# Kernel optimization log

Hardware: AMD Instinct MI355X
Metric: run time of the kernel (lower is better)

## Reference

```python
import math
import jax, jax.numpy as jnp
import numpy as np

NTYPE, C, H, E = 3, 256, 8, 32  # n_embd=256, n_head=8, edge_dim=32
A1 = 16  # aux_x1 feature dim (aux_x2 dim = E - A1)


def setup_inputs() -> dict:
    key = jax.random.key(0)
    ks = jax.random.split(key, 16)
    B, T1, T2 = 8, 128, 256
    s = 0.02
    return {
        "x1": jax.random.normal(ks[0], (B, T1, C), jnp.float32),
        "x2": jax.random.normal(ks[1], (B, T2, C), jnp.float32),
        "aux_x1": jax.random.normal(ks[2], (B, T1, A1), jnp.float32),
        "aux_x2": jax.random.normal(ks[3], (B, T2, E - A1), jnp.float32),
        "masks": jax.random.randint(ks[4], (NTYPE, B, T1, T2), 0, 2, jnp.int32),
        # per-type linear params, stored (in, out) so y = x @ W + b
        "Wq": jax.random.normal(ks[5], (NTYPE, C, C), jnp.float32) * s,
        "bq": jnp.zeros((NTYPE, C), jnp.float32),
        "Wk": jax.random.normal(ks[6], (NTYPE, C + E, C), jnp.float32) * s,
        "bk": jnp.zeros((NTYPE, C), jnp.float32),
        "Wv": jax.random.normal(ks[7], (NTYPE, C + E, C), jnp.float32) * s,
        "bv": jnp.zeros((NTYPE, C), jnp.float32),
        "Wp": jax.random.normal(ks[8], (NTYPE, C, C), jnp.float32) * s,
        "bp": jnp.zeros((NTYPE, C), jnp.float32),
    }


def _aux_attn(x1, x2, aux_x1, aux_x2, mask, Wq, bq, Wk, bk, Wv, bv, Wp, bp):
    """One AuxCrossAttention type. mask: (B,T1,T2) int."""
    B, T1, _ = x1.shape
    T2 = x2.shape[1]
    hd = C // H
    scale = 1.0 / math.sqrt(hd)

    q = x1 @ Wq + bq  # (B,T1,C)
    # k/v over aug_x2 = [x2 | aux_x1 | aux_x2]; split the linear instead of
    # materializing the (B,T1,T2,C+E) concat (same math by linearity).
    Wk_x, Wk_a1, Wk_a2 = Wk[:C], Wk[C:C + A1], Wk[C + A1:]
    Wv_x, Wv_a1, Wv_a2 = Wv[:C], Wv[C:C + A1], Wv[C + A1:]
    k = (x2 @ Wk_x + aux_x2 @ Wk_a2 + bk)[:, None] + (aux_x1 @ Wk_a1)[:, :, None]  # (B,T1,T2,C)
    v = (x2 @ Wv_x + aux_x2 @ Wv_a2 + bv)[:, None] + (aux_x1 @ Wv_a1)[:, :, None]  # (B,T1,T2,C)

    qh = q.reshape(B, T1, H, hd)
    kh = k.reshape(B, T1, T2, H, hd)
    vh = v.reshape(B, T1, T2, H, hd)

    att = jnp.einsum("bthd,btshd->bhts", qh, kh) * scale  # (B,H,T1,T2)
    valid = (mask != 0)[:, None]  # (B,1,T1,T2)
    att = jnp.where(valid, att, -jnp.inf)
    all_masked = (mask == 0).all(-1)  # (B,T1)
    att = jnp.where(all_masked[:, None, :, None], 0.0, att)
    f = jnp.finfo(att.dtype)
    att = jnp.nan_to_num(att, nan=0.0, posinf=f.max, neginf=f.min)
    att = jax.nn.softmax(att, axis=-1)

    y = jnp.einsum("bhts,btshd->bthd", att, vh).reshape(B, T1, C)
    return y @ Wp + bp


def reference(x1, x2, aux_x1, aux_x2, masks, Wq, bq, Wk, bk, Wv, bv, Wp, bp):
    resid = jnp.zeros_like(x1)
    for i in range(NTYPE):
        resid = resid + _aux_attn(x1, x2, aux_x1, aux_x2, masks[i],
                                  Wq[i], bq[i], Wk[i], bk[i], Wv[i], bv[i], Wp[i], bp[i])
    return resid
```

## Files before the change

kernel.cpp:

```cpp
#include <hip/hip_runtime.h>
#include <hip/hip_bf16.h>

#define NC 256
#define HD 32

typedef __attribute__((ext_vector_type(8))) short short8;
typedef __attribute__((ext_vector_type(4))) short short4v;
typedef __attribute__((ext_vector_type(4))) float f32x4;

#define QSC (0.17677669529663687f * 1.4426950408889634f)

__device__ __forceinline__ unsigned short f2bf(float f) {
    union { float f; unsigned u; } v; v.f = f;
    unsigned r = v.u + 0x7fffu + ((v.u >> 16) & 1u);
    return (unsigned short)(r >> 16);
}
__device__ __forceinline__ short8 cvt8(float4 a, float4 b) {
    short8 s;
    s[0] = (short)f2bf(a.x); s[1] = (short)f2bf(a.y);
    s[2] = (short)f2bf(a.z); s[3] = (short)f2bf(a.w);
    s[4] = (short)f2bf(b.x); s[5] = (short)f2bf(b.y);
    s[6] = (short)f2bf(b.z); s[7] = (short)f2bf(b.w);
    return s;
}

__global__ __launch_bounds__(256) void prep(
    const float* __restrict__ x1, const float* __restrict__ x2,
    const float* __restrict__ ax1, const float* __restrict__ ax2,
    const int* __restrict__ masks,
    const float* __restrict__ Wq, const float* __restrict__ Wk,
    const float* __restrict__ Wv, const float* __restrict__ Wp,
    short* __restrict__ x1b, short* __restrict__ A2, short* __restrict__ ax1p,
    unsigned int* __restrict__ mb,
    short* __restrict__ WqT, short* __restrict__ WkT, short* __restrict__ WvT,
    short* __restrict__ WpT)
{
    const int bx = blockIdx.x, tid = threadIdx.x;
    const short8 zero8 = {0, 0, 0, 0, 0, 0, 0, 0};

    if (bx < 64) {
        const size_t base = ((size_t)bx * 256 + tid) * 16;
        const float* p = x1 + base;
        float4 a = *(const float4*)p,       b = *(const float4*)(p + 4);
        float4 c = *(const float4*)(p + 8), d = *(const float4*)(p + 12);
        *(short8*)&x1b[base]     = cvt8(a, b);
        *(short8*)&x1b[base + 8] = cvt8(c, d);
    } else if (bx < 352) {
        const int g = (bx - 64) * 256 + tid;
        const int row = g / 36, c8 = g - row * 36;
        short8 s;
        if (c8 < 32) {
            const float* p = x2 + (size_t)row * 256 + c8 * 8;
            s = cvt8(*(const float4*)p, *(const float4*)(p + 4));
        } else if (c8 < 34) {
            const float* p = ax2 + (size_t)row * 16 + (c8 - 32) * 8;
            s = cvt8(*(const float4*)p, *(const float4*)(p + 4));
        } else {
            s = zero8;
        }
        *(short8*)&A2[(size_t)row * 288 + c8 * 8] = s;
    } else if (bx < 356) {
        const int row = (bx - 352) * 256 + tid;
        const float* p = ax1 + (size_t)row * 16;
        float4 a = *(const float4*)p,       b = *(const float4*)(p + 4);
        float4 c = *(const float4*)(p + 8), d = *(const float4*)(p + 12);
        short* o = ax1p + (size_t)row * 32;
        *(short8*)o        = cvt8(a, b);
        *(short8*)(o + 8)  = cvt8(c, d);
        *(short8*)(o + 16) = zero8;
        *(short8*)(o + 24) = zero8;
    } else if (bx < 548) {
        const int r0 = (bx - 356) * 16;
        const int wave = tid >> 6, lane = tid & 63;
        for (int rr = 0; rr < 16; ++rr) {
            const int row = r0 + rr;
            const int mk = masks[(size_t)row * 256 + tid];
            unsigned long long bal = __ballot(mk != 0);
            if (lane == 0) {
                mb[row * 8 + wave * 2 + 0] = (unsigned int)bal;
                mb[row * 8 + wave * 2 + 1] = (unsigned int)(bal >> 32);
            }
        }
    } else if (bx < 644) {
        const int idx = bx - 548, i = idx >> 5, k8 = idx & 31;
        const int n = tid;
        const float* W = Wq + (size_t)i * 256 * 256;
        short8 s;
#pragma unroll
        for (int j = 0; j < 8; ++j) s[j] = (short)f2bf(W[(size_t)(k8 * 8 + j) * 256 + n]);
        *(short8*)&WqT[(size_t)i * 256 * 256 + (size_t)n * 256 + k8 * 8] = s;
    } else if (bx < 860) {
        const int idx0 = bx - 644;
        const int kv = idx0 / 108, idx = idx0 % 108;
        const int i = idx / 36, k8 = idx % 36;
        const int n = tid;
        const float* W = (kv ? Wv : Wk) + (size_t)i * 288 * 256;
        short* O = (kv ? WvT : WkT) + (size_t)i * 256 * 288;
        short8 s;
#pragma unroll
        for (int j = 0; j < 8; ++j) {
            const int kp = k8 * 8 + j;
            const int src = (kp < 256) ? kp : (kp < 272 ? kp + 16 : -1);
            s[j] = (src >= 0) ? (short)f2bf(W[(size_t)src * 256 + n]) : (short)0;
        }
        *(short8*)&O[(size_t)n * 288 + k8 * 8] = s;
    } else {
        const int idx = bx - 860, i = idx >> 5, k8 = idx & 31;
        const int n = tid;
        const float* W = Wp + (size_t)i * 256 * 256;
        short8 s;
#pragma unroll
        for (int j = 0; j < 8; ++j) s[j] = (short)f2bf(W[(size_t)(k8 * 8 + j) * 256 + n]);
        *(short8*)&WpT[(size_t)i * 256 * 256 + (size_t)n * 256 + k8 * 8] = s;
    }
}

__global__ __launch_bounds__(1024) void qkv_attn(
    const short* __restrict__ x1b, const short* __restrict__ A2,
    const short* __restrict__ WqT, const short* __restrict__ WkT,
    const short* __restrict__ WvT, const float* __restrict__ Wv,
    const short* __restrict__ WpT,
    const float* __restrict__ bq, const float* __restrict__ bk,
    const float* __restrict__ bv, const unsigned int* __restrict__ mb,
    short* __restrict__ yb, short* __restrict__ WeffT)
{
    const int tid = threadIdx.x;
    const int wave = tid >> 6, lane = tid & 63;
    const int qd = lane >> 4, ml = lane & 15;
    const int bx = blockIdx.x;

    if (bx >= 192) {
        if (wave != 0) return;
        const int wb = bx - 192;
        const int n = wb * 16 + ml;
        f32x4 acc = {0.f, 0.f, 0.f, 0.f};
        for (int i = 0; i < 3; ++i) {
            const float* Wvp = Wv + (size_t)i * 288 * 256;
            const short* Wpt = WpT + (size_t)i * 256 * 256;
#pragma unroll
            for (int step = 0; step < 8; ++step) {
                const float* ap = Wvp + (size_t)(256 + ml) * 256 + step * 32 + qd * 8;
                short8 af = cvt8(*(const float4*)ap, *(const float4*)(ap + 4));
                short8 bf = *(const short8*)&Wpt[(size_t)n * 256 + step * 32 + qd * 8];
                acc = __builtin_amdgcn_mfma_f32_16x16x32_bf16(af, bf, acc, 0, 0, 0);
            }
        }
#pragma unroll
        for (int r = 0; r < 4; ++r) {
            WeffT[n * 32 + qd * 4 + r] = (short)f2bf(acc[r]);
            WeffT[n * 32 + 16 + qd * 4 + r] = 0;
        }
        return;
    }

    const int i = bx >> 6, b = (bx >> 3) & 7, h = bx & 7;
    const size_t bb = (size_t)i * 8 + b;
    const int hc = h * 32;

    __shared__ short q_s[128][40];
    __shared__ short k_s[256][40];
    __shared__ short vT_s[32][264];
    __shared__ short P_s[8][1024];

    const short* Wq_i = WqT + (size_t)i * 256 * 256;
    const short* Wk_i = WkT + (size_t)i * 256 * 288;
    const short* Wv_i = WvT + (size_t)i * 256 * 288;

    f32x4 qacc[2], kacc[2], vacc[2];
#pragma unroll
    for (int nt = 0; nt < 2; ++nt) {
        qacc[nt] = {0.f, 0.f, 0.f, 0.f};
        kacc[nt] = {0.f, 0.f, 0.f, 0.f};
        vacc[nt] = {0.f, 0.f, 0.f, 0.f};
    }

    for (int step = 0; step < 8; ++step) {
        short8 afq, bfq[2], af, bfk[2], bfv[2];
        if (wave < 8) {
            afq = *(const short8*)&x1b[(size_t)(b * 128 + wave * 16 + ml) * 256 + step * 32 + qd * 8];
#pragma unroll
            for (int nt = 0; nt < 2; ++nt)
                bfq[nt] = *(const short8*)&Wq_i[(size_t)(hc + nt * 16 + ml) * 256 + step * 32 + qd * 8];
        }
        af = *(const short8*)&A2[(size_t)(b * 256 + wave * 16 + ml) * 288 + step * 32 + qd * 8];
#pragma unroll
        for (int nt = 0; nt < 2; ++nt) {
            bfk[nt] = *(const short8*)&Wk_i[(size_t)(hc + nt * 16 + ml) * 288 + step * 32 + qd * 8];
            bfv[nt] = *(const short8*)&Wv_i[(size_t)(hc + nt * 16 + ml) * 288 + step * 32 + qd * 8];
        }
        if (wave < 8) {
#pragma unroll
            for (int nt = 0; nt < 2; ++nt)
                qacc[nt] = __builtin_amdgcn_mfma_f32_16x16x32_bf16(afq, bfq[nt], qacc[nt], 0, 0, 0);
        }
#pragma unroll
        for (int nt = 0; nt < 2; ++nt) {
            kacc[nt] = __builtin_amdgcn_mfma_f32_16x16x32_bf16(af, bfk[nt], kacc[nt], 0, 0, 0);
            vacc[nt] = __builtin_amdgcn_mfma_f32_16x16x32_bf16(af, bfv[nt], vacc[nt], 0, 0, 0);
        }
    }
    {
        const int step = 8;
        short8 af, bfk[2], bfv[2];
        af = *(const short8*)&A2[(size_t)(b * 256 + wave * 16 + ml) * 288 + step * 32 + qd * 8];
#pragma unroll
        for (int nt = 0; nt < 2; ++nt) {
            bfk[nt] = *(const short8*)&Wk_i[(size_t)(hc + nt * 16 + ml) * 288 + step * 32 + qd * 8];
            bfv[nt] = *(const short8*)&Wv_i[(size_t)(hc + nt * 16 + ml) * 288 + step * 32 + qd * 8];
        }
#pragma unroll
        for (int nt = 0; nt < 2; ++nt) {
            kacc[nt] = __builtin_amdgcn_mfma_f32_16x16x32_bf16(af, bfk[nt], kacc[nt], 0, 0, 0);
            vacc[nt] = __builtin_amdgcn_mfma_f32_16x16x32_bf16(af, bfv[nt], vacc[nt], 0, 0, 0);
        }
    }

    if (wave < 8) {
#pragma unroll
        for (int nt = 0; nt < 2; ++nt) {
            const float bsq = bq[i * 256 + hc + nt * 16 + ml];
            const int r0 = wave * 16 + qd * 4;
#pragma unroll
            for (int r = 0; r < 4; ++r)
                q_s[r0 + r][nt * 16 + ml] = (short)f2bf((qacc[nt][r] + bsq) * QSC);
        }
    }
#pragma unroll
    for (int nt = 0; nt < 2; ++nt) {
        const float bsk = bk[i * 256 + hc + nt * 16 + ml];
        const float bsvv = bv[i * 256 + hc + nt * 16 + ml];
        const int s0 = wave * 16 + qd * 4;
#pragma unroll
        for (int r = 0; r < 4; ++r)
            k_s[s0 + r][nt * 16 + ml] = (short)f2bf(kacc[nt][r] + bsk);
        short4v s;
        s.x = (short)f2bf(vacc[nt][0] + bsvv);
        s.y = (short)f2bf(vacc[nt][1] + bsvv);
        s.z = (short)f2bf(vacc[nt][2] + bsvv);
        s.w = (short)f2bf(vacc[nt][3] + bsvv);
        *(short4v*)&vT_s[nt * 16 + ml][s0] = s;
    }
    __syncthreads();

    if (wave >= 8) return;
    short* Pw = &P_s[wave][0];
    {
        const int t0 = wave * 16;
        const int tb = t0 + qd * 4;

        uint4 wlo[4], whi[4];
#pragma unroll
        for (int r = 0; r < 4; ++r) {
            const unsigned int* p = mb + (bb * 128 + tb + r) * 8;
            wlo[r] = *(const uint4*)p;
            whi[r] = *(const uint4*)(p + 4);
        }

        short8 af = *(const short8*)&q_s[t0 + ml][qd * 8];

        f32x4 sacc[16];
#pragma unroll
        for (int nt = 0; nt < 16; ++nt) sacc[nt] = {0.f, 0.f, 0.f, 0.f};
#pragma unroll
        for (int nt = 0; nt < 16; ++nt) {
            short8 bf = *(const short8*)&k_s[nt * 16 + ml][qd * 8];
            sacc[nt] = __builtin_amdgcn_mfma_f32_16x16x32_bf16(af, bf, sacc[nt], 0, 0, 0);
        }

        f32x4 rs = {0.f, 0.f, 0.f, 0.f};
#pragma unroll
        for (int nt = 0; nt < 16; ++nt) {
#pragma unroll
            for (int r = 0; r < 4; ++r) {
                unsigned int w;
                switch (nt >> 1) {
                    case 0: w = wlo[r].x; break; case 1: w = wlo[r].y; break;
                    case 2: w = wlo[r].z; break; case 3: w = wlo[r].w; break;
                    case 4: w = whi[r].x; break; case 5: w = whi[r].y; break;
                    case 6: w = whi[r].z; break; default: w = whi[r].w; break;
                }
                const bool mk = (w >> ((nt & 1) * 16 + ml)) & 1u;
                float e = mk ? __builtin_amdgcn_exp2f(sacc[nt][r]) : 0.f;
                sacc[nt][r] = e;
                rs[r] += e;
            }
        }
#pragma unroll
        for (int off = 1; off <= 8; off <<= 1) {
#pragma unroll
            for (int r = 0; r < 4; ++r) rs[r] += __shfl_xor(rs[r], off);
        }
        f32x4 pinv, pfill;
#pragma unroll
        for (int r = 0; r < 4; ++r) {
            const bool z = (rs[r] == 0.f);
            pinv[r]  = z ? 0.f : 1.f / rs[r];
            pfill[r] = z ? (1.f / 256.f) : 0.f;
        }

        f32x4 oacc[2];
        oacc[0] = {0.f, 0.f, 0.f, 0.f};
        oacc[1] = {0.f, 0.f, 0.f, 0.f};
#pragma unroll
        for (int quar = 0; quar < 4; ++quar) {
#pragma unroll
            for (int nt4 = 0; nt4 < 4; ++nt4) {
                const int nt = quar * 4 + nt4;
                const int sgrp = 2 * nt4 + (ml >> 3);
                const int pos = ml & 7;
#pragma unroll
                for (int r = 0; r < 4; ++r) {
                    const float p = sacc[nt][r] * pinv[r] + pfill[r];
                    Pw[(sgrp * 16 + qd * 4 + r) * 8 + pos] = (short)f2bf(p);
                }
            }
#pragma unroll
            for (int ksl = 0; ksl < 2; ++ksl) {
                const int ks = quar * 2 + ksl;
                short8 pa = *(const short8*)&Pw[((ksl * 4 + qd) * 16 + ml) * 8];
#pragma unroll
                for (int n2 = 0; n2 < 2; ++n2) {
                    short8 vf = *(const short8*)&vT_s[n2 * 16 + ml][ks * 32 + qd * 8];
                    oacc[n2] = __builtin_amdgcn_mfma_f32_16x16x32_bf16(pa, vf, oacc[n2], 0, 0, 0);
                }
            }
        }

#pragma unroll
        for (int n2 = 0; n2 < 2; ++n2) {
            const int d = hc + n2 * 16 + ml;
#pragma unroll
            for (int r = 0; r < 4; ++r)
                yb[(size_t)(bb * 128 + tb + r) * 256 + d] = (short)f2bf(oacc[n2][r]);
        }
    }
}

__global__ __launch_bounds__(256) void proj2(
    const short* __restrict__ yb, const short* __restrict__ WpT,
    const short* __restrict__ ax1p, const short* __restrict__ WeffT,
    const float* __restrict__ bp, float* __restrict__ out)
{
    const int bx = blockIdx.x;
    const int m0 = (bx >> 2) * 16, n0 = (bx & 3) * 64;
    const int tid = threadIdx.x;
    const int wave = tid >> 6, lane = tid & 63;
    const int qd = lane >> 4, ml = lane & 15;
    const int col = n0 + wave * 16 + ml;

    f32x4 acc = {0.f, 0.f, 0.f, 0.f};

#pragma unroll
    for (int i = 0; i < 3; ++i) {
        const short* A = yb + (size_t)i * 1024 * 256;
        const short* W = WpT + (size_t)i * 256 * 256;
#pragma unroll
        for (int step = 0; step < 8; ++step) {
            short8 af = *(const short8*)&A[(size_t)(m0 + ml) * 256 + step * 32 + qd * 8];
            short8 bf = *(const short8*)&W[(size_t)col * 256 + step * 32 + qd * 8];
            acc = __builtin_amdgcn_mfma_f32_16x16x32_bf16(af, bf, acc, 0, 0, 0);
        }
    }
    {
        short8 af = *(const short8*)&ax1p[(size_t)(m0 + ml) * 32 + qd * 8];
        short8 bf = *(const short8*)&WeffT[(size_t)col * 32 + qd * 8];
        acc = __builtin_amdgcn_mfma_f32_16x16x32_bf16(af, bf, acc, 0, 0, 0);
    }
    const float b3 = bp[col] + bp[256 + col] + bp[512 + col];
    const int row0 = m0 + qd * 4;
#pragma unroll
    for (int r = 0; r < 4; ++r)
        out[(size_t)(row0 + r) * 256 + col] = acc[r] + b3;
}

extern "C" void kernel_launch(void* const* d_in, const int* in_sizes, int n_in,
                              void* d_out, int out_size, void* d_ws, size_t ws_size,
                              hipStream_t stream)
{
    const float* x1  = (const float*)d_in[0];
    const float* x2  = (const float*)d_in[1];
    const float* ax1 = (const float*)d_in[2];
    const float* ax2 = (const float*)d_in[3];
    const int*   mk  = (const int*)d_in[4];
    const float* Wq  = (const float*)d_in[5];
    const float* bq  = (const float*)d_in[6];
    const float* Wk  = (const float*)d_in[7];
    const float* bk  = (const float*)d_in[8];
    const float* Wv  = (const float*)d_in[9];
    const float* bv  = (const float*)d_in[10];
    const float* Wp  = (const float*)d_in[11];
    const float* bp  = (const float*)d_in[12];

    char* w = (char*)d_ws;
    short* x1b   = (short*)(w + 0);
    short* A2    = (short*)(w + 524288);
    short* ax1p  = (short*)(w + 1703936);
    short* WqT   = (short*)(w + 1769472);
    short* WkT   = (short*)(w + 2162688);
    short* WvT   = (short*)(w + 2605056);
    short* WpT   = (short*)(w + 3047424);
    unsigned int* mbits = (unsigned int*)(w + 3440640);
    short* WeffT = (short*)(w + 3538944);
    short* yb    = (short*)(w + 3555328);

    prep<<<dim3(956), 256, 0, stream>>>(x1, x2, ax1, ax2, mk, Wq, Wk, Wv, Wp,
                                        x1b, A2, ax1p, mbits, WqT, WkT, WvT, WpT);
    qkv_attn<<<dim3(208), 1024, 0, stream>>>(x1b, A2, WqT, WkT, WvT, Wv, WpT,
                                             bq, bk, bv, mbits, yb, WeffT);
    proj2<<<dim3(256), 256, 0, stream>>>(yb, WpT, ax1p, WeffT, bp, (float*)d_out);
}
```

Measured before the change: 116.5 us.

## Fuse fp32-to-bf16 conversion of activations and Q/K/V weights into qkv_attn

```diff
diff --git a/kernel.cpp b/kernel.cpp
--- a/kernel.cpp
+++ b/kernel.cpp
@@ -23,44 +23,54 @@
     s[6] = (short)f2bf(b.z); s[7] = (short)f2bf(b.w);
     return s;
 }
+__device__ __forceinline__ short8 wfrag(const float* __restrict__ W, int k0, int n) {
+    short8 s;
+#pragma unroll
+    for (int j = 0; j < 8; ++j) s[j] = (short)f2bf(W[(size_t)(k0 + j) * 256 + n]);
+    return s;
+}
+__device__ __forceinline__ short8 wfrag288(const float* __restrict__ W, int k0, int n) {
+    short8 s;
+#pragma unroll
+    for (int j = 0; j < 8; ++j) {
+        const int kp = k0 + j;
+        const int src = (kp < 256) ? kp : (kp < 272 ? kp + 16 : -1);
+        s[j] = (src >= 0) ? (short)f2bf(W[(size_t)src * 256 + n]) : (short)0;
+    }
+    return s;
+}
 
 __global__ __launch_bounds__(256) void prep(
-    const float* __restrict__ x1, const float* __restrict__ x2,
-    const float* __restrict__ ax1, const float* __restrict__ ax2,
-    const int* __restrict__ masks,
-    const float* __restrict__ Wq, const float* __restrict__ Wk,
-    const float* __restrict__ Wv, const float* __restrict__ Wp,
-    short* __restrict__ x1b, short* __restrict__ A2, short* __restrict__ ax1p,
-    unsigned int* __restrict__ mb,
-    short* __restrict__ WqT, short* __restrict__ WkT, short* __restrict__ WvT,
-    short* __restrict__ WpT)
+    const int* __restrict__ masks, const float* __restrict__ Wp,
+    const float* __restrict__ ax1,
+    unsigned int* __restrict__ mb, short* __restrict__ WpT,
+    short* __restrict__ ax1p)
 {
     const int bx = blockIdx.x, tid = threadIdx.x;
     const short8 zero8 = {0, 0, 0, 0, 0, 0, 0, 0};
 
-    if (bx < 64) {
-        const size_t base = ((size_t)bx * 256 + tid) * 16;
-        const float* p = x1 + base;
-        float4 a = *(const float4*)p,       b = *(const float4*)(p + 4);
-        float4 c = *(const float4*)(p + 8), d = *(const float4*)(p + 12);
-        *(short8*)&x1b[base]     = cvt8(a, b);
-        *(short8*)&x1b[base + 8] = cvt8(c, d);
-    } else if (bx < 352) {
-        const int g = (bx - 64) * 256 + tid;
-        const int row = g / 36, c8 = g - row * 36;
+    if (bx < 192) {
+        const int r0 = bx * 16;
+        const int wave = tid >> 6, lane = tid & 63;
+        for (int rr = 0; rr < 16; ++rr) {
+            const int row = r0 + rr;
+            const int mk = masks[(size_t)row * 256 + tid];
+            unsigned long long bal = __ballot(mk != 0);
+            if (lane == 0) {
+                mb[row * 8 + wave * 2 + 0] = (unsigned int)bal;
+                mb[row * 8 + wave * 2 + 1] = (unsigned int)(bal >> 32);
+            }
+        }
+    } else if (bx < 288) {
+        const int idx = bx - 192, i = idx >> 5, k8 = idx & 31;
+        const int n = tid;
+        const float* W = Wp + (size_t)i * 256 * 256;
         short8 s;
-        if (c8 < 32) {
-            const float* p = x2 + (size_t)row * 256 + c8 * 8;
-            s = cvt8(*(const float4*)p, *(const float4*)(p + 4));
-        } else if (c8 < 34) {
-            const float* p = ax2 + (size_t)row * 16 + (c8 - 32) * 8;
-            s = cvt8(*(const float4*)p, *(const float4*)(p + 4));
-        } else {
-            s = zero8;
-        }
-        *(short8*)&A2[(size_t)row * 288 + c8 * 8] = s;
-    } else if (bx < 356) {
-        const int row = (bx - 352) * 256 + tid;
+#pragma unroll
+        for (int j = 0; j < 8; ++j) s[j] = (short)f2bf(W[(size_t)(k8 * 8 + j) * 256 + n]);
+        *(short8*)&WpT[(size_t)i * 256 * 256 + (size_t)n * 256 + k8 * 8] = s;
+    } else {
+        const int row = (bx - 288) * 256 + tid;
         const float* p = ax1 + (size_t)row * 16;
         float4 a = *(const float4*)p,       b = *(const float4*)(p + 4);
         float4 c = *(const float4*)(p + 8), d = *(const float4*)(p + 12);
@@ -69,57 +79,14 @@
         *(short8*)(o + 8)  = cvt8(c, d);
         *(short8*)(o + 16) = zero8;
         *(short8*)(o + 24) = zero8;
-    } else if (bx < 548) {
-        const int r0 = (bx - 356) * 16;
-        const int wave = tid >> 6, lane = tid & 63;
-        for (int rr = 0; rr < 16; ++rr) {
-            const int row = r0 + rr;
-            const int mk = masks[(size_t)row * 256 + tid];
-            unsigned long long bal = __ballot(mk != 0);
-            if (lane == 0) {
-                mb[row * 8 + wave * 2 + 0] = (unsigned int)bal;
-                mb[row * 8 + wave * 2 + 1] = (unsigned int)(bal >> 32);
-            }
-        }
-    } else if (bx < 644) {
-        const int idx = bx - 548, i = idx >> 5, k8 = idx & 31;
-        const int n = tid;
-        const float* W = Wq + (size_t)i * 256 * 256;
-        short8 s;
-#pragma unroll
-        for (int j = 0; j < 8; ++j) s[j] = (short)f2bf(W[(size_t)(k8 * 8 + j) * 256 + n]);
-        *(short8*)&WqT[(size_t)i * 256 * 256 + (size_t)n * 256 + k8 * 8] = s;
-    } else if (bx < 860) {
-        const int idx0 = bx - 644;
-        const int kv = idx0 / 108, idx = idx0 % 108;
-        const int i = idx / 36, k8 = idx % 36;
-        const int n = tid;
-        const float* W = (kv ? Wv : Wk) + (size_t)i * 288 * 256;
-        short* O = (kv ? WvT : WkT) + (size_t)i * 256 * 288;
-        short8 s;
-#pragma unroll
-        for (int j = 0; j < 8; ++j) {
-            const int kp = k8 * 8 + j;
-            const int src = (kp < 256) ? kp : (kp < 272 ? kp + 16 : -1);
-            s[j] = (src >= 0) ? (short)f2bf(W[(size_t)src * 256 + n]) : (short)0;
-        }
-        *(short8*)&O[(size_t)n * 288 + k8 * 8] = s;
-    } else {
-        const int idx = bx - 860, i = idx >> 5, k8 = idx & 31;
-        const int n = tid;
-        const float* W = Wp + (size_t)i * 256 * 256;
-        short8 s;
-#pragma unroll
-        for (int j = 0; j < 8; ++j) s[j] = (short)f2bf(W[(size_t)(k8 * 8 + j) * 256 + n]);
-        *(short8*)&WpT[(size_t)i * 256 * 256 + (size_t)n * 256 + k8 * 8] = s;
     }
 }
 
 __global__ __launch_bounds__(1024) void qkv_attn(
-    const short* __restrict__ x1b, const short* __restrict__ A2,
-    const short* __restrict__ WqT, const short* __restrict__ WkT,
-    const short* __restrict__ WvT, const float* __restrict__ Wv,
-    const short* __restrict__ WpT,
+    const float* __restrict__ x1, const float* __restrict__ x2,
+    const float* __restrict__ ax2,
+    const float* __restrict__ Wq, const float* __restrict__ Wk,
+    const float* __restrict__ Wv, const short* __restrict__ WpT,
     const float* __restrict__ bq, const float* __restrict__ bk,
     const float* __restrict__ bv, const unsigned int* __restrict__ mb,
     short* __restrict__ yb, short* __restrict__ WeffT)
@@ -128,6 +95,7 @@
     const int wave = tid >> 6, lane = tid & 63;
     const int qd = lane >> 4, ml = lane & 15;
     const int bx = blockIdx.x;
+    const short8 zero8 = {0, 0, 0, 0, 0, 0, 0, 0};
 
     if (bx >= 192) {
         if (wave != 0) return;
@@ -162,9 +130,9 @@
     __shared__ short vT_s[32][264];
     __shared__ short P_s[8][1024];
 
-    const short* Wq_i = WqT + (size_t)i * 256 * 256;
-    const short* Wk_i = WkT + (size_t)i * 256 * 288;
-    const short* Wv_i = WvT + (size_t)i * 256 * 288;
+    const float* Wq_i = Wq + (size_t)i * 256 * 256;
+    const float* Wk_i = Wk + (size_t)i * 288 * 256;
+    const float* Wv_i = Wv + (size_t)i * 288 * 256;
 
     f32x4 qacc[2], kacc[2], vacc[2];
 #pragma unroll
@@ -175,18 +143,23 @@
     }
 
     for (int step = 0; step < 8; ++step) {
+        const int k0 = step * 32 + qd * 8;
         short8 afq, bfq[2], af, bfk[2], bfv[2];
         if (wave < 8) {
-            afq = *(const short8*)&x1b[(size_t)(b * 128 + wave * 16 + ml) * 256 + step * 32 + qd * 8];
+            const float* px = x1 + (size_t)(b * 128 + wave * 16 + ml) * 256 + k0;
+            afq = cvt8(*(const float4*)px, *(const float4*)(px + 4));
 #pragma unroll
             for (int nt = 0; nt < 2; ++nt)
-                bfq[nt] = *(const short8*)&Wq_i[(size_t)(hc + nt * 16 + ml) * 256 + step * 32 + qd * 8];
-        }
-        af = *(const short8*)&A2[(size_t)(b * 256 + wave * 16 + ml) * 288 + step * 32 + qd * 8];
-#pragma unroll
-        for (int nt = 0; nt < 2; ++nt) {
-            bfk[nt] = *(const short8*)&Wk_i[(size_t)(hc + nt * 16 + ml) * 288 + step * 32 + qd * 8];
-            bfv[nt] = *(const short8*)&Wv_i[(size_t)(hc + nt * 16 + ml) * 288 + step * 32 + qd * 8];
+                bfq[nt] = wfrag(Wq_i, k0, hc + nt * 16 + ml);
+        }
+        {
+            const float* pa = x2 + (size_t)(b * 256 + wave * 16 + ml) * 256 + k0;
+            af = cvt8(*(const float4*)pa, *(const float4*)(pa + 4));
+        }
+#pragma unroll
+        for (int nt = 0; nt < 2; ++nt) {
+            bfk[nt] = wfrag288(Wk_i, k0, hc + nt * 16 + ml);
+            bfv[nt] = wfrag288(Wv_i, k0, hc + nt * 16 + ml);
         }
         if (wave < 8) {
 #pragma unroll
@@ -200,13 +173,18 @@
         }
     }
     {
-        const int step = 8;
+        const int k0 = 256 + qd * 8;
         short8 af, bfk[2], bfv[2];
-        af = *(const short8*)&A2[(size_t)(b * 256 + wave * 16 + ml) * 288 + step * 32 + qd * 8];
-#pragma unroll
-        for (int nt = 0; nt < 2; ++nt) {
-            bfk[nt] = *(const short8*)&Wk_i[(size_t)(hc + nt * 16 + ml) * 288 + step * 32 + qd * 8];
-            bfv[nt] = *(const short8*)&Wv_i[(size_t)(hc + nt * 16 + ml) * 288 + step * 32 + qd * 8];
+        if (qd < 2) {
+            const float* pa = ax2 + (size_t)(b * 256 + wave * 16 + ml) * 16 + qd * 8;
+            af = cvt8(*(const float4*)pa, *(const float4*)(pa + 4));
+        } else {
+            af = zero8;
+        }
+#pragma unroll
+        for (int nt = 0; nt < 2; ++nt) {
+            bfk[nt] = wfrag288(Wk_i, k0, hc + nt * 16 + ml);
+            bfv[nt] = wfrag288(Wv_i, k0, hc + nt * 16 + ml);
         }
 #pragma unroll
         for (int nt = 0; nt < 2; ++nt) {
@@ -392,20 +370,14 @@
     const float* bp  = (const float*)d_in[12];
 
     char* w = (char*)d_ws;
-    short* x1b   = (short*)(w + 0);
-    short* A2    = (short*)(w + 524288);
     short* ax1p  = (short*)(w + 1703936);
-    short* WqT   = (short*)(w + 1769472);
-    short* WkT   = (short*)(w + 2162688);
-    short* WvT   = (short*)(w + 2605056);
     short* WpT   = (short*)(w + 3047424);
     unsigned int* mbits = (unsigned int*)(w + 3440640);
     short* WeffT = (short*)(w + 3538944);
     short* yb    = (short*)(w + 3555328);
 
-    prep<<<dim3(956), 256, 0, stream>>>(x1, x2, ax1, ax2, mk, Wq, Wk, Wv, Wp,
-                                        x1b, A2, ax1p, mbits, WqT, WkT, WvT, WpT);
-    qkv_attn<<<dim3(208), 1024, 0, stream>>>(x1b, A2, WqT, WkT, WvT, Wv, WpT,
+    prep<<<dim3(292), 256, 0, stream>>>(mk, Wp, ax1, mbits, WpT, ax1p);
+    qkv_attn<<<dim3(208), 1024, 0, stream>>>(x1, x2, ax2, Wq, Wk, Wv, WpT,
                                              bq, bk, bv, mbits, yb, WeffT);
     proj2<<<dim3(256), 256, 0, stream>>>(yb, WpT, ax1p, WeffT, bp, (float*)d_out);
 }
```

After: 123.3 us. 5.8% more time.
